# Kernel optimization log

Measured on AMD Instinct MI355X. Metric: run time of the kernel, lower is better.

## Reference

```python
import jax, jax.numpy as jnp
import numpy as np

N_EMBD = 1024
N_HEAD = 16
HEAD_SIZE = N_EMBD // N_HEAD  # 64
ROPE_BASE = 10000.0


def apply_rope(x, pos):
    # x: [B, T, H, D] (torchtune layout), interleaved-pair rotation
    D = x.shape[-1]
    theta = 1.0 / (ROPE_BASE ** (jnp.arange(0, D, 2, dtype=jnp.float32) / D))  # [D/2]
    ang = pos.astype(jnp.float32)[:, None] * theta[None, :]                    # [T, D/2]
    cos = jnp.cos(ang)[None, :, None, :].astype(x.dtype)
    sin = jnp.sin(ang)[None, :, None, :].astype(x.dtype)
    xr = x.reshape(*x.shape[:-1], D // 2, 2)
    x0, x1 = xr[..., 0], xr[..., 1]
    out = jnp.stack([x0 * cos - x1 * sin, x1 * cos + x0 * sin], axis=-1)
    return out.reshape(x.shape)


def setup_inputs() -> dict:
    key = jax.random.key(0)
    k1, k2, k3 = jax.random.split(key, 3)
    B, T = 4, 1000
    x = jax.random.normal(k1, (B, T, N_EMBD), dtype=jnp.float32)
    # causal boolean mask (True = attend), as passed to F.scaled_dot_product_attention
    attn_mask = jnp.tril(jnp.ones((T, T), dtype=bool))[None, None, :, :]
    # Linear weights stored as [in, out] (i.e. torch weight transposed), fan-in scaled
    W_attn = jax.random.normal(k2, (N_EMBD, 3 * N_EMBD), dtype=jnp.float32) * (1.0 / np.sqrt(N_EMBD))
    W_proj = jax.random.normal(k3, (N_EMBD, N_EMBD), dtype=jnp.float32) * (1.0 / np.sqrt(N_EMBD))
    return {"x": x, "attn_mask": attn_mask, "W_attn": W_attn, "W_proj": W_proj}


def reference(x, attn_mask, W_attn, W_proj):
    B, T, C = x.shape
    qkv = x @ W_attn                                   # [B, T, 3C]
    q, k, v = jnp.split(qkv, 3, axis=-1)
    q = q.reshape(B, T, N_HEAD, HEAD_SIZE)
    k = k.reshape(B, T, N_HEAD, HEAD_SIZE)
    v = v.reshape(B, T, N_HEAD, HEAD_SIZE)
    pos = jnp.arange(T)
    q = apply_rope(q, pos)
    k = apply_rope(k, pos)
    # causal SDPA (dropout = 0)
    scale = 1.0 / np.sqrt(HEAD_SIZE)
    scores = jnp.einsum('bqhd,bkhd->bhqk', q, k) * scale   # [B, H, T, T]
    neg = jnp.asarray(jnp.finfo(scores.dtype).min, scores.dtype)
    scores = jnp.where(attn_mask, scores, neg)
    probs = jax.nn.softmax(scores, axis=-1)
    y = jnp.einsum('bhqk,bkhd->bqhd', probs, v)             # [B, T, H, D]
    y = y.reshape(B, T, C)
    return y @ W_proj
```

## Files before the change

kernel.cpp:

```cpp
#include <hip/hip_runtime.h>

typedef unsigned short ushortT;
typedef unsigned int uintT;
typedef __attribute__((ext_vector_type(8))) short bf16x8;
typedef __attribute__((ext_vector_type(4))) float f32x4;

#define B_ 4
#define T_ 1000
#define H_ 16
#define MP 4096
#define QSCALE 0.18033688011112042f

__device__ __forceinline__ ushortT f2bf(float f) {
    unsigned u = __float_as_uint(f);
    u += 0x7fffu + ((u >> 16) & 1u);
    return (ushortT)(u >> 16);
}
__device__ __forceinline__ float fast_exp2(float x) {
#if __has_builtin(__builtin_amdgcn_exp2f)
    return __builtin_amdgcn_exp2f(x);
#else
    return exp2f(x);
#endif
}

__global__ void prep_kernel(const float* __restrict__ x,
                            const float* __restrict__ Wa, const float* __restrict__ Wp,
                            ushortT* __restrict__ Xb,
                            ushortT* __restrict__ Wat, ushortT* __restrict__ Wpt) {
    __shared__ float tile[64][65];
    int bid = blockIdx.x, tid = threadIdx.x;
    if (bid < 4096) {
        int e = (bid * 256 + tid) * 4;
        int r = e >> 10, col = e & 1023;
        int b = r >> 10, t = r & 1023;
        ushort4 o = make_ushort4(0, 0, 0, 0);
        if (t < T_) {
            float4 v = *(const float4*)(x + (((size_t)(b * T_ + t)) << 10) + col);
            o.x = f2bf(v.x); o.y = f2bf(v.y); o.z = f2bf(v.z); o.w = f2bf(v.w);
        }
        *(ushort4*)(Xb + (size_t)e) = o;
        return;
    }
    const float* W; ushortT* Wt; int N, bx, by;
    if (bid < 4096 + 768) { W = Wa; Wt = Wat; N = 3072; int id = bid - 4096; bx = id % 48; by = id / 48; }
    else                  { W = Wp; Wt = Wpt; N = 1024; int id = bid - 4864; bx = id & 15; by = id >> 4; }
    int k0 = by * 64, n0 = bx * 64;
    int lane = tid & 63, w4 = tid >> 6;
#pragma unroll 4
    for (int i = 0; i < 16; ++i) {
        int row = i * 4 + w4;
        tile[row][lane] = W[(size_t)(k0 + row) * N + n0 + lane];
    }
    __syncthreads();
#pragma unroll 4
    for (int i = 0; i < 16; ++i) {
        int row = i * 4 + w4;
        Wt[(size_t)(n0 + row) * 1024 + k0 + lane] = f2bf(tile[lane][row]);
    }
}

__global__ __launch_bounds__(256, 2) void gemm_qkv_kernel(
    const ushortT* __restrict__ A, const ushortT* __restrict__ Bt,
    ushortT* __restrict__ Qb, ushortT* __restrict__ Kb, ushortT* __restrict__ Vtb)
{
    __shared__ __align__(16) ushortT smem[16896];
    ushortT* As = smem;
    ushortT* Bs = smem + 8192;
    const int K = 1024;
    int tid = threadIdx.x, wave = tid >> 6, lane = tid & 63;
    int m0 = blockIdx.y * 128, n0 = blockIdx.x * 128;
    int wm = (wave >> 1) * 64, wn = (wave & 1) * 64;
    int col0 = lane & 15, quad = lane >> 4;

    f32x4 acc[4][4] = {};

    for (int kt = 0; kt < 16; ++kt) {
        int k0 = kt * 64;
        __syncthreads();
#pragma unroll
        for (int it = 0; it < 4; ++it) {
            int gci = (wave * 4 + it) * 64 + lane;
            int r = gci >> 3, c = gci & 7;
            int sc = c ^ (r & 7);
            const ushortT* ga = A + (size_t)(m0 + r) * K + k0 + sc * 8;
            __builtin_amdgcn_global_load_lds(
                (const __attribute__((address_space(1))) unsigned int*)ga,
                (__attribute__((address_space(3))) unsigned int*)(As + (wave * 4 + it) * 512),
                16, 0, 0);
            const ushortT* gb = Bt + (size_t)(n0 + r) * K + k0 + sc * 8;
            __builtin_amdgcn_global_load_lds(
                (const __attribute__((address_space(1))) unsigned int*)gb,
                (__attribute__((address_space(3))) unsigned int*)(Bs + (wave * 4 + it) * 512),
                16, 0, 0);
        }
        __syncthreads();
#pragma unroll
        for (int s = 0; s < 2; ++s) {
            int g = s * 4 + quad;
            bf16x8 af[4], bfr[4];
#pragma unroll
            for (int mi = 0; mi < 4; ++mi) {
                int r = wm + mi * 16 + col0;
                af[mi] = *(const bf16x8*)(As + r * 64 + ((g ^ (r & 7)) * 8));
            }
#pragma unroll
            for (int ni = 0; ni < 4; ++ni) {
                int r = wn + ni * 16 + col0;
                bfr[ni] = *(const bf16x8*)(Bs + r * 64 + ((g ^ (r & 7)) * 8));
            }
#pragma unroll
            for (int mi = 0; mi < 4; ++mi)
#pragma unroll
                for (int ni = 0; ni < 4; ++ni)
                    acc[mi][ni] = __builtin_amdgcn_mfma_f32_16x16x32_bf16(
                        af[mi], bfr[ni], acc[mi][ni], 0, 0, 0);
        }
    }
    __syncthreads();

    int sec = n0 >> 10, cb = n0 & 1023;
    int b = m0 >> 10, tbase = m0 & 1023;

    if (sec < 2) {
        float2* tab = (float2*)smem;
#pragma unroll
        for (int i = 0; i < 16; ++i) {
            int task = i * 256 + tid;
            int tl = task >> 5, p = task & 31;
            float theta = __expf(-(float)p * 0.28782313662425572f);
            float ang = (float)(tbase + tl) * theta;
            float sn, cs;
            sincosf(ang, &sn, &cs);
            tab[tl * 33 + p] = make_float2(cs, sn);
        }
        __syncthreads();
        ushortT* Out = sec ? Kb : Qb;
        float qs = sec ? 1.0f : QSCALE;
#pragma unroll
        for (int mi = 0; mi < 4; ++mi) {
#pragma unroll
            for (int j = 0; j < 4; ++j) {
                int tl = wm + mi * 16 + quad * 4 + j;
                int t = tbase + tl;
                bool valid = t < T_;
#pragma unroll
                for (int nt = 0; nt < 4; ++nt) {
                    float xv = acc[mi][nt][j];
                    float xp = __shfl_xor(xv, 1);
                    int cl = wn + nt * 16 + col0;
                    int d = cl & 63;
                    float2 cssn = tab[tl * 33 + (d >> 1)];
                    float r = (d & 1) ? (xv * cssn.x + xp * cssn.y)
                                      : (xv * cssn.x - xp * cssn.y);
                    r *= qs;
                    if (valid)
                        Out[((size_t)((b << 4) | ((cb + cl) >> 6)) << 16) + (t << 6) + d] = f2bf(r);
                }
            }
        }
    } else {
        ushortT* Ls = smem;
#pragma unroll
        for (int mi = 0; mi < 4; ++mi) {
#pragma unroll
            for (int nt = 0; nt < 4; ++nt) {
                int cl = wn + nt * 16 + col0;
                int rb = wm + mi * 16 + quad * 4;
                uintT lo = (uintT)f2bf(acc[mi][nt][0]) | ((uintT)f2bf(acc[mi][nt][1]) << 16);
                uintT hi = (uintT)f2bf(acc[mi][nt][2]) | ((uintT)f2bf(acc[mi][nt][3]) << 16);
                *(uint2*)(Ls + cl * 132 + rb) = make_uint2(lo, hi);
            }
        }
        __syncthreads();
#pragma unroll
        for (int it = 0; it < 8; ++it) {
            int u = it * 256 + tid;
            int cl = u >> 4, c = u & 15;
            int d = cl & 63, h = (cb + cl) >> 6;
            ushortT tmp[8];
#pragma unroll
            for (int j = 0; j < 8; ++j) tmp[j] = Ls[cl * 132 + j * 16 + c];
            *(bf16x8*)(Vtb + (((size_t)((b << 4) | h)) << 16) + ((size_t)d << 10) + tbase + c * 8)
                = *(bf16x8*)tmp;
        }
    }
}

#define PSTR 136
template <bool LAST>
__device__ __forceinline__ void softmax_store(f32x4* sc4, ushortT* Ps,
                                              int wave, int quad, int col0,
                                              int q0, int j0) {
#pragma unroll
    for (int reg = 0; reg < 4; ++reg) {
        int m = quad * 4 + reg;
        int q = q0 + wave * 16 + m;
        float pv[8];
#pragma unroll
        for (int nt = 0; nt < 8; ++nt) {
            float p = fast_exp2(sc4[nt][reg]);
            if (LAST && (j0 + nt * 16 + col0) > q) p = 0.f;
            pv[nt] = p;
        }
        int4 pk;
        pk.x = __builtin_amdgcn_perm(__float_as_uint(pv[1]), __float_as_uint(pv[0]), 0x07060302u);
        pk.y = __builtin_amdgcn_perm(__float_as_uint(pv[3]), __float_as_uint(pv[2]), 0x07060302u);
        pk.z = __builtin_amdgcn_perm(__float_as_uint(pv[5]), __float_as_uint(pv[4]), 0x07060302u);
        pk.w = __builtin_amdgcn_perm(__float_as_uint(pv[7]), __float_as_uint(pv[6]), 0x07060302u);
        *(int4*)(Ps + (wave * 16 + m) * PSTR + col0 * 8) = pk;
    }
}

__global__ __launch_bounds__(256, 3) void attn_mfma_kernel(
    const ushortT* __restrict__ Qb, const ushortT* __restrict__ Kb,
    const ushortT* __restrict__ Vtb, ushortT* __restrict__ Yb)
{
    __shared__ __align__(16) ushortT Ks[128 * 64];
    __shared__ __align__(16) ushortT Vs[64 * 128];
    __shared__ __align__(16) ushortT Ps[64 * PSTR];

    int bh = blockIdx.x;
    int b = bh >> 4, h = bh & 15;
    int qi = 15 - blockIdx.y;
    int q0 = qi * 64;
    int tid = threadIdx.x, wave = tid >> 6, lane = tid & 63;
    int col0 = lane & 15, quad = lane >> 4;

    const ushortT* Kbh  = Kb  + ((size_t)bh << 16);
    const ushortT* Vtbh = Vtb + ((size_t)bh << 16);

    const ushortT* qrowp = Qb + ((size_t)bh << 16) + (size_t)(q0 + wave * 16 + col0) * 64;
    bf16x8 aq[2];
    aq[0] = *(const bf16x8*)(qrowp + quad * 8);
    aq[1] = *(const bf16x8*)(qrowp + 32 + quad * 8);

    bf16x8 onesb;
#pragma unroll
    for (int i = 0; i < 8; ++i) onesb[i] = (short)0x3F80;

    f32x4 o[4] = {};
    f32x4 lsum = {};

    int nchunks = qi / 2 + 1;
    for (int cc = 0; cc < nchunks; ++cc) {
        int j0 = cc * 128;
        __syncthreads();
#pragma unroll
        for (int it = 0; it < 4; ++it) {
            int gci = (wave * 4 + it) * 64 + lane;
            {
                int r = gci >> 3, c = gci & 7;
                int sc = c ^ (r & 7);
                const ushortT* gk = Kbh + (size_t)(j0 + r) * 64 + sc * 8;
                __builtin_amdgcn_global_load_lds(
                    (const __attribute__((address_space(1))) unsigned int*)gk,
                    (__attribute__((address_space(3))) unsigned int*)(Ks + (wave * 4 + it) * 512),
                    16, 0, 0);
            }
            {
                int d = gci >> 4, c = gci & 15;
                int sc = c ^ (d & 15);
                const ushortT* gv = Vtbh + (size_t)d * 1024 + j0 + sc * 8;
                __builtin_amdgcn_global_load_lds(
                    (const __attribute__((address_space(1))) unsigned int*)gv,
                    (__attribute__((address_space(3))) unsigned int*)(Vs + (wave * 4 + it) * 512),
                    16, 0, 0);
            }
        }
        __syncthreads();

        f32x4 sc4[8] = {};
#pragma unroll
        for (int s = 0; s < 2; ++s) {
#pragma unroll
            for (int nt = 0; nt < 8; ++nt) {
                int r = nt * 16 + col0;
                bf16x8 bk = *(const bf16x8*)(Ks + r * 64 + (((s * 4 + quad) ^ (col0 & 7)) * 8));
                sc4[nt] = __builtin_amdgcn_mfma_f32_16x16x32_bf16(aq[s], bk, sc4[nt], 0, 0, 0);
            }
        }

        if (cc == nchunks - 1)
            softmax_store<true>(sc4, Ps, wave, quad, col0, q0, j0);
        else
            softmax_store<false>(sc4, Ps, wave, quad, col0, q0, j0);

#pragma unroll
        for (int s = 0; s < 4; ++s) {
            bf16x8 ap = *(const bf16x8*)(Ps + (wave * 16 + col0) * PSTR + s * 32 + quad * 8);
            lsum = __builtin_amdgcn_mfma_f32_16x16x32_bf16(ap, onesb, lsum, 0, 0, 0);
#pragma unroll
            for (int nt = 0; nt < 4; ++nt) {
                int d = nt * 16 + col0;
                bf16x8 bv = *(const bf16x8*)(Vs + d * 128 + (((s * 4 + quad) ^ col0) * 8));
                o[nt] = __builtin_amdgcn_mfma_f32_16x16x32_bf16(ap, bv, o[nt], 0, 0, 0);
            }
        }
    }

#pragma unroll
    for (int reg = 0; reg < 4; ++reg) {
        int q = q0 + wave * 16 + quad * 4 + reg;
        if (q < T_) {
            float inv_l = 1.0f / lsum[reg];
            ushortT* yp = Yb + ((size_t)(b * 1024 + q) << 10) + h * 64;
#pragma unroll
            for (int nt = 0; nt < 4; ++nt)
                yp[nt * 16 + col0] = f2bf(o[nt][reg] * inv_l);
        }
    }
}

__global__ __launch_bounds__(256, 3) void gemm_proj_kernel(
    const ushortT* __restrict__ A, const ushortT* __restrict__ Bt,
    float* __restrict__ Cout)
{
    __shared__ __align__(16) ushortT As[64 * 64];
    __shared__ __align__(16) ushortT Bs[128 * 64];
    const int K = 1024;
    int tid = threadIdx.x, wave = tid >> 6, lane = tid & 63;
    int m0 = blockIdx.y * 64, n0 = blockIdx.x * 128;
    int wm = (wave >> 1) * 32, wn = (wave & 1) * 64;
    int col0 = lane & 15, quad = lane >> 4;

    f32x4 acc[2][4] = {};

    for (int kt = 0; kt < 16; ++kt) {
        int k0 = kt * 64;
        __syncthreads();
#pragma unroll
        for (int it = 0; it < 2; ++it) {
            int gci = it * 256 + tid;
            int r = gci >> 3, c = gci & 7;
            int sc = c ^ (r & 7);
            const ushortT* ga = A + (size_t)(m0 + r) * K + k0 + sc * 8;
            __builtin_amdgcn_global_load_lds(
                (const __attribute__((address_space(1))) unsigned int*)ga,
                (__attribute__((address_space(3))) unsigned int*)(As + it * 2048 + wave * 512),
                16, 0, 0);
        }
#pragma unroll
        for (int it = 0; it < 4; ++it) {
            int gci = it * 256 + tid;
            int r = gci >> 3, c = gci & 7;
            int sc = c ^ (r & 7);
            const ushortT* gb = Bt + (size_t)(n0 + r) * K + k0 + sc * 8;
            __builtin_amdgcn_global_load_lds(
                (const __attribute__((address_space(1))) unsigned int*)gb,
                (__attribute__((address_space(3))) unsigned int*)(Bs + it * 2048 + wave * 512),
                16, 0, 0);
        }
        __syncthreads();
#pragma unroll
        for (int s = 0; s < 2; ++s) {
            int g = s * 4 + quad;
            bf16x8 af[2], bfr[4];
#pragma unroll
            for (int mi = 0; mi < 2; ++mi) {
                int r = wm + mi * 16 + col0;
                af[mi] = *(const bf16x8*)(As + r * 64 + ((g ^ (r & 7)) * 8));
            }
#pragma unroll
            for (int ni = 0; ni < 4; ++ni) {
                int r = wn + ni * 16 + col0;
                bfr[ni] = *(const bf16x8*)(Bs + r * 64 + ((g ^ (r & 7)) * 8));
            }
#pragma unroll
            for (int mi = 0; mi < 2; ++mi)
#pragma unroll
                for (int ni = 0; ni < 4; ++ni)
                    acc[mi][ni] = __builtin_amdgcn_mfma_f32_16x16x32_bf16(
                        af[mi], bfr[ni], acc[mi][ni], 0, 0, 0);
        }
    }

#pragma unroll
    for (int mi = 0; mi < 2; ++mi) {
#pragma unroll
        for (int j = 0; j < 4; ++j) {
            int row = m0 + wm + mi * 16 + quad * 4 + j;
            int t = row & 1023, b = row >> 10;
            if (t < T_) {
                float* cp = Cout + ((size_t)(b * T_ + t) << 10) + n0 + wn;
#pragma unroll
                for (int ni = 0; ni < 4; ++ni)
                    cp[ni * 16 + col0] = acc[mi][ni][j];
            }
        }
    }
}

extern "C" void kernel_launch(void* const* d_in, const int* in_sizes, int n_in,
                              void* d_out, int out_size, void* d_ws, size_t ws_size,
                              hipStream_t stream) {
    const float* x      = (const float*)d_in[0];
    const float* W_attn = (const float*)d_in[2];
    const float* W_proj = (const float*)d_in[3];
    float* out = (float*)d_out;

    uintptr_t w = (uintptr_t)d_ws;
    ushortT* Xb  = (ushortT*)(w);
    ushortT* Wat = (ushortT*)(w + 8388608);
    ushortT* Wpt = (ushortT*)(w + 14680064);
    ushortT* Qb  = (ushortT*)(w + 16777216);
    ushortT* Kb  = (ushortT*)(w + 25165824);
    ushortT* Vtb = (ushortT*)(w + 33554432);
    ushortT* Yb  = (ushortT*)(w + 41943040);

    prep_kernel<<<dim3(5120), dim3(256), 0, stream>>>(x, W_attn, W_proj, Xb, Wat, Wpt);

    gemm_qkv_kernel<<<dim3(24, 32), dim3(256), 0, stream>>>(Xb, Wat, Qb, Kb, Vtb);

    attn_mfma_kernel<<<dim3(64, 16), dim3(256), 0, stream>>>(Qb, Kb, Vtb, Yb);

    gemm_proj_kernel<<<dim3(8, 64), dim3(256), 0, stream>>>(Yb, Wpt, out);
}
```

Baseline: 155.3 us.

## Process 128 query rows per attention block to reuse staged K/V tiles

The attention kernel now handles two 64-row query sub-tiles per block, so each K/V chunk loaded into shared memory serves 128 queries and global K/V traffic is halved. The grid shrinks to 8 query tiles per head and the P buffer doubles, so the occupancy hint drops from 3 to 2 blocks. The QKV GEMM occupancy hint is raised from 2 to 3, which may constrain registers. Fewer, larger blocks add more causal imbalance and waste, since the diagonal chunk is now masked for a 128-row tile.

```diff
diff --git a/kernel.cpp b/kernel.cpp
--- a/kernel.cpp
+++ b/kernel.cpp
@@ -60,7 +60,7 @@
     }
 }
 
-__global__ __launch_bounds__(256, 2) void gemm_qkv_kernel(
+__global__ __launch_bounds__(256, 3) void gemm_qkv_kernel(
     const ushortT* __restrict__ A, const ushortT* __restrict__ Bt,
     ushortT* __restrict__ Qb, ushortT* __restrict__ Kb, ushortT* __restrict__ Vtb)
 {
@@ -191,11 +191,11 @@
 template <bool LAST>
 __device__ __forceinline__ void softmax_store(f32x4* sc4, ushortT* Ps,
                                               int wave, int quad, int col0,
-                                              int q0, int j0) {
+                                              int qrow0, int j0) {
 #pragma unroll
     for (int reg = 0; reg < 4; ++reg) {
         int m = quad * 4 + reg;
-        int q = q0 + wave * 16 + m;
+        int q = qrow0 + m;
         float pv[8];
 #pragma unroll
         for (int nt = 0; nt < 8; ++nt) {
@@ -212,37 +212,41 @@
     }
 }
 
-__global__ __launch_bounds__(256, 3) void attn_mfma_kernel(
+__global__ __launch_bounds__(256, 2) void attn_mfma_kernel(
     const ushortT* __restrict__ Qb, const ushortT* __restrict__ Kb,
     const ushortT* __restrict__ Vtb, ushortT* __restrict__ Yb)
 {
     __shared__ __align__(16) ushortT Ks[128 * 64];
     __shared__ __align__(16) ushortT Vs[64 * 128];
-    __shared__ __align__(16) ushortT Ps[64 * PSTR];
+    __shared__ __align__(16) ushortT Ps[128 * PSTR];
 
     int bh = blockIdx.x;
     int b = bh >> 4, h = bh & 15;
-    int qi = 15 - blockIdx.y;
-    int q0 = qi * 64;
+    int qi = 7 - blockIdx.y;
+    int q0 = qi * 128;
     int tid = threadIdx.x, wave = tid >> 6, lane = tid & 63;
     int col0 = lane & 15, quad = lane >> 4;
 
     const ushortT* Kbh  = Kb  + ((size_t)bh << 16);
     const ushortT* Vtbh = Vtb + ((size_t)bh << 16);
 
-    const ushortT* qrowp = Qb + ((size_t)bh << 16) + (size_t)(q0 + wave * 16 + col0) * 64;
-    bf16x8 aq[2];
-    aq[0] = *(const bf16x8*)(qrowp + quad * 8);
-    aq[1] = *(const bf16x8*)(qrowp + 32 + quad * 8);
+    bf16x8 aq[2][2];
+#pragma unroll
+    for (int u = 0; u < 2; ++u) {
+        const ushortT* qrowp = Qb + ((size_t)bh << 16)
+                             + (size_t)(q0 + u * 64 + wave * 16 + col0) * 64;
+        aq[u][0] = *(const bf16x8*)(qrowp + quad * 8);
+        aq[u][1] = *(const bf16x8*)(qrowp + 32 + quad * 8);
+    }
 
     bf16x8 onesb;
 #pragma unroll
     for (int i = 0; i < 8; ++i) onesb[i] = (short)0x3F80;
 
-    f32x4 o[4] = {};
-    f32x4 lsum = {};
-
-    int nchunks = qi / 2 + 1;
+    f32x4 o[2][4] = {};
+    f32x4 lsum[2] = {};
+
+    int nchunks = qi + 1;
     for (int cc = 0; cc < nchunks; ++cc) {
         int j0 = cc * 128;
         __syncthreads();
@@ -270,44 +274,52 @@
         }
         __syncthreads();
 
-        f32x4 sc4[8] = {};
-#pragma unroll
-        for (int s = 0; s < 2; ++s) {
-#pragma unroll
-            for (int nt = 0; nt < 8; ++nt) {
-                int r = nt * 16 + col0;
-                bf16x8 bk = *(const bf16x8*)(Ks + r * 64 + (((s * 4 + quad) ^ (col0 & 7)) * 8));
-                sc4[nt] = __builtin_amdgcn_mfma_f32_16x16x32_bf16(aq[s], bk, sc4[nt], 0, 0, 0);
-            }
-        }
-
-        if (cc == nchunks - 1)
-            softmax_store<true>(sc4, Ps, wave, quad, col0, q0, j0);
-        else
-            softmax_store<false>(sc4, Ps, wave, quad, col0, q0, j0);
-
-#pragma unroll
-        for (int s = 0; s < 4; ++s) {
-            bf16x8 ap = *(const bf16x8*)(Ps + (wave * 16 + col0) * PSTR + s * 32 + quad * 8);
-            lsum = __builtin_amdgcn_mfma_f32_16x16x32_bf16(ap, onesb, lsum, 0, 0, 0);
-#pragma unroll
-            for (int nt = 0; nt < 4; ++nt) {
-                int d = nt * 16 + col0;
-                bf16x8 bv = *(const bf16x8*)(Vs + d * 128 + (((s * 4 + quad) ^ col0) * 8));
-                o[nt] = __builtin_amdgcn_mfma_f32_16x16x32_bf16(ap, bv, o[nt], 0, 0, 0);
-            }
-        }
-    }
-
-#pragma unroll
-    for (int reg = 0; reg < 4; ++reg) {
-        int q = q0 + wave * 16 + quad * 4 + reg;
-        if (q < T_) {
-            float inv_l = 1.0f / lsum[reg];
-            ushortT* yp = Yb + ((size_t)(b * 1024 + q) << 10) + h * 64;
-#pragma unroll
-            for (int nt = 0; nt < 4; ++nt)
-                yp[nt * 16 + col0] = f2bf(o[nt][reg] * inv_l);
+        bool last = (cc == nchunks - 1);
+#pragma unroll
+        for (int u = 0; u < 2; ++u) {
+            f32x4 sc4[8] = {};
+#pragma unroll
+            for (int s = 0; s < 2; ++s) {
+#pragma unroll
+                for (int nt = 0; nt < 8; ++nt) {
+                    int r = nt * 16 + col0;
+                    bf16x8 bk = *(const bf16x8*)(Ks + r * 64 + (((s * 4 + quad) ^ (col0 & 7)) * 8));
+                    sc4[nt] = __builtin_amdgcn_mfma_f32_16x16x32_bf16(aq[u][s], bk, sc4[nt], 0, 0, 0);
+                }
+            }
+            ushortT* Psu = Ps + u * 64 * PSTR;
+            int qrow0 = q0 + u * 64 + wave * 16;
+            if (last)
+                softmax_store<true>(sc4, Psu, wave, quad, col0, qrow0, j0);
+            else
+                softmax_store<false>(sc4, Psu, wave, quad, col0, qrow0, j0);
+
+#pragma unroll
+            for (int s = 0; s < 4; ++s) {
+                bf16x8 ap = *(const bf16x8*)(Psu + (wave * 16 + col0) * PSTR + s * 32 + quad * 8);
+                lsum[u] = __builtin_amdgcn_mfma_f32_16x16x32_bf16(ap, onesb, lsum[u], 0, 0, 0);
+#pragma unroll
+                for (int nt = 0; nt < 4; ++nt) {
+                    int d = nt * 16 + col0;
+                    bf16x8 bv = *(const bf16x8*)(Vs + d * 128 + (((s * 4 + quad) ^ col0) * 8));
+                    o[u][nt] = __builtin_amdgcn_mfma_f32_16x16x32_bf16(ap, bv, o[u][nt], 0, 0, 0);
+                }
+            }
+        }
+    }
+
+#pragma unroll
+    for (int u = 0; u < 2; ++u) {
+#pragma unroll
+        for (int reg = 0; reg < 4; ++reg) {
+            int q = q0 + u * 64 + wave * 16 + quad * 4 + reg;
+            if (q < T_) {
+                float inv_l = 1.0f / lsum[u][reg];
+                ushortT* yp = Yb + ((size_t)(b * 1024 + q) << 10) + h * 64;
+#pragma unroll
+                for (int nt = 0; nt < 4; ++nt)
+                    yp[nt * 16 + col0] = f2bf(o[u][nt][reg] * inv_l);
+            }
         }
     }
 }
@@ -412,7 +424,7 @@
 
     gemm_qkv_kernel<<<dim3(24, 32), dim3(256), 0, stream>>>(Xb, Wat, Qb, Kb, Vtb);
 
-    attn_mfma_kernel<<<dim3(64, 16), dim3(256), 0, stream>>>(Qb, Kb, Vtb, Yb);
+    attn_mfma_kernel<<<dim3(64, 8), dim3(256), 0, stream>>>(Qb, Kb, Vtb, Yb);
 
     gemm_proj_kernel<<<dim3(8, 64), dim3(256), 0, stream>>>(Yb, Wpt, out);
 }
```

Result: slower. 163.6 us (+5.4%).
